# Kernel optimization log

Measured on AMD Instinct MI355X. Metric: run time of the kernel, lower is better.

The kernel has to match this reference:

```python
import jax, jax.numpy as jnp
import numpy as np
from jax import lax

STRIDE = (1, 1)
PADDING = ((1, 1), (1, 1))  # stride=1, padding=1 for 3x3 conv


def setup_inputs() -> dict:
    key = jax.random.key(0)
    k1, k2 = jax.random.split(key)
    x = jax.random.normal(k1, (16, 32, 224, 224), dtype=jnp.float32)
    # kaiming_normal_(mode='fan_out', nonlinearity='relu'): std = sqrt(2/fan_out)
    fan_out = 32 * 3 * 3
    weight = jax.random.normal(k2, (32, 32, 3, 3), dtype=jnp.float32) * np.sqrt(2.0 / fan_out)
    return {"x": x, "weight": weight}


def reference(x, weight):
    # absmax 8-bit activation fake-quant
    x_scale = jnp.abs(x).max() + 1e-5
    x_q = jnp.round(jnp.clip(x * 127.0 / x_scale, -128.0, 127.0))
    # BitNet b1.58 ternary weight fake-quant
    w_scale = jnp.abs(weight).mean() + 1e-5
    w_q = jnp.clip(jnp.round(weight / w_scale), -1.0, 1.0)
    # straight-through estimator (no-op in pure forward, kept for fidelity)
    w_ste = weight + lax.stop_gradient(w_q * w_scale - weight)
    x_ste = x + lax.stop_gradient(x_q * (x_scale / 127.0) - x)
    out = lax.conv_general_dilated(
        x_ste, w_ste,
        window_strides=STRIDE,
        padding=PADDING,
        dimension_numbers=("NCHW", "OIHW", "NCHW"),
    )
    return out
```

## Files before the change

kernel.cpp:

```cpp
#include <hip/hip_runtime.h>


typedef __attribute__((ext_vector_type(8))) short short8;
typedef __attribute__((ext_vector_type(4))) float f32x4;

#define HW    224
#define NCH   32
#define PLANE (HW * HW)
#define TH 16
#define TW 32

__device__ __forceinline__ int lds_h(int pix, int c) {
    int sw = (pix & 3) ^ ((pix >> 2) & 3);
    return pix * 32 + (c & 7) + ((((c >> 3) ^ sw) & 3) << 3);
}


__global__ __launch_bounds__(256) void absmax_kernel(const float* __restrict__ x,
                                                     unsigned* __restrict__ slots, int n4)
{
    const float4* x4 = (const float4*)x;
    float m = 0.f;
    int stride = gridDim.x * blockDim.x;
    for (int i = blockIdx.x * blockDim.x + threadIdx.x; i < n4; i += stride) {
        float4 v = x4[i];
        m = fmaxf(m, fmaxf(fmaxf(fabsf(v.x), fabsf(v.y)),
                           fmaxf(fabsf(v.z), fabsf(v.w))));
    }
    #pragma unroll
    for (int off = 32; off > 0; off >>= 1)
        m = fmaxf(m, __shfl_xor(m, off));
    __shared__ float wm[4];
    int lane = threadIdx.x & 63, wv = threadIdx.x >> 6;
    if (lane == 0) wm[wv] = m;
    __syncthreads();
    if (threadIdx.x == 0) {
        m = fmaxf(fmaxf(wm[0], wm[1]), fmaxf(wm[2], wm[3]));
        slots[blockIdx.x] = __float_as_uint(m);
    }
}

__global__ __launch_bounds__(256) void prep_kernel(const float* __restrict__ w,
                                                   const unsigned* __restrict__ slots,
                                                   float* __restrict__ scal,
                                                   unsigned short* __restrict__ wbuf)
{
    float s = 0.f;
    for (int i = threadIdx.x; i < 9216; i += 256) s += fabsf(w[i]);
    float m = 0.f;
    for (int i = threadIdx.x; i < 2048; i += 256)
        m = fmaxf(m, __uint_as_float(slots[i]));
    #pragma unroll
    for (int off = 32; off > 0; off >>= 1) {
        s += __shfl_xor(s, off);
        m = fmaxf(m, __shfl_xor(m, off));
    }
    __shared__ float sm[4], mm[4];
    __shared__ float s_ws;
    int lane = threadIdx.x & 63, wv = threadIdx.x >> 6;
    if (lane == 0) { sm[wv] = s; mm[wv] = m; }
    __syncthreads();
    if (threadIdx.x == 0) {
        float wscale = (sm[0] + sm[1] + sm[2] + sm[3]) / 9216.f + 1e-5f;
        float xscale = fmaxf(fmaxf(mm[0], mm[1]), fmaxf(mm[2], mm[3])) + 1e-5f;
        scal[0] = (xscale / 127.f) * wscale;
        scal[1] = 127.f / xscale;
        s_ws = wscale;
    }
    __syncthreads();
    float wscale = s_ws;
    for (int o = threadIdx.x; o < 9216; o += 256) {
        int frag = o >> 9, rem = o & 511;
        int l = rem >> 3, j = rem & 7;
        int tap = frag >> 1, kb = frag & 1;
        int kout = kb * 16 + (l & 15);
        int c = ((l >> 4) << 3) + j;
        int r = tap / 3, ss = tap % 3;
        float wv2 = w[((kout * 32 + c) * 3 + r) * 3 + ss];
        float q = fminf(1.f, fmaxf(-1.f, rintf(wv2 / wscale)));
        wbuf[o] = (unsigned short)(__float_as_uint(q) >> 16);
    }
}

__global__ __launch_bounds__(512, 4) void conv_kernel(const float* __restrict__ x,
                                                      const unsigned short* __restrict__ wbuf,
                                                      const float* __restrict__ scal,
                                                      float* __restrict__ out)
{
    __shared__ __align__(16) unsigned short xs[612 * 32];

    int bid = (blockIdx.x & 7) * 196 + (blockIdx.x >> 3);
    int tw = bid % 7;
    int rest = bid / 7;
    int th = rest % 14;
    int n  = rest / 14;
    int h0 = th * TH, w0 = tw * TW;

    int tid = threadIdx.x;
    int lane = tid & 63, wv = tid >> 6;

    float inv = scal[1];
    const float* xn = x + n * (NCH * PLANE);

    const short8* wfp = (const short8*)wbuf;
    short8 wa = wfp[lane];
    short8 wb = wfp[64 + lane];

    int slot = tid & 7;
    int c = (tid >> 3) & 31;
    int half = tid >> 8;
    const float* tb = xn + c * PLANE + w0 + slot * 4;
    int pixb = 1 + slot * 4;
    int hbase = half * 9;

    float4 v[9];
    float invr[9];
    #pragma unroll
    for (int i = 0; i < 9; ++i) {
        int gh = h0 - 1 + hbase + i;
        int ghc = gh < 0 ? 0 : (gh > HW - 1 ? HW - 1 : gh);
        invr[i] = (gh == ghc) ? inv : 0.f;
        v[i] = *(const float4*)(tb + ghc * HW);
    }
    float hv[3];
    #pragma unroll
    for (int it = 0; it < 3; ++it) {
        int e = tid + it * 512;
        hv[it] = 0.f;
        if (e < 1152) {
            int side = e & 1;
            int cc = (e >> 1) & 31;
            int hp = e >> 6;
            int gh = h0 - 1 + hp;
            int gw = side ? (w0 + TW) : (w0 - 1);
            int ghc = gh < 0 ? 0 : (gh > HW - 1 ? HW - 1 : gh);
            int gwc = gw < 0 ? 0 : (gw > HW - 1 ? HW - 1 : gw);
            float vv = xn[cc * PLANE + ghc * HW + gwc];
            hv[it] = (gh == ghc && gw == gwc) ? vv * inv : 0.f;
        }
    }
    #pragma unroll
    for (int i = 0; i < 9; ++i) {
        int p0 = (hbase + i) * 34 + pixb;
        float q0 = rintf(fminf(127.f, fmaxf(-128.f, v[i].x * invr[i])));
        float q1 = rintf(fminf(127.f, fmaxf(-128.f, v[i].y * invr[i])));
        float q2 = rintf(fminf(127.f, fmaxf(-128.f, v[i].z * invr[i])));
        float q3 = rintf(fminf(127.f, fmaxf(-128.f, v[i].w * invr[i])));
        xs[lds_h(p0 + 0, c)] = (unsigned short)(__float_as_uint(q0) >> 16);
        xs[lds_h(p0 + 1, c)] = (unsigned short)(__float_as_uint(q1) >> 16);
        xs[lds_h(p0 + 2, c)] = (unsigned short)(__float_as_uint(q2) >> 16);
        xs[lds_h(p0 + 3, c)] = (unsigned short)(__float_as_uint(q3) >> 16);
    }
    #pragma unroll
    for (int it = 0; it < 3; ++it) {
        int e = tid + it * 512;
        if (e < 1152) {
            int side = e & 1;
            int cc = (e >> 1) & 31;
            int hp = e >> 6;
            float q = rintf(fminf(127.f, fmaxf(-128.f, hv[it])));
            xs[lds_h(hp * 34 + (side ? 33 : 0), cc)] =
                (unsigned short)(__float_as_uint(q) >> 16);
        }
    }
    __syncthreads();

    int ln = lane & 15, cb = lane >> 4;
    f32x4 acc[2][2][2] = {};

    for (int tap = 0; tap < 9; ++tap) {
        short8 na, nb;
        if (tap < 8) {
            na = wfp[(2 * tap + 2) * 64 + lane];
            nb = wfp[(2 * tap + 3) * 64 + lane];
        }
        int r = tap / 3;
        int s2 = tap - r * 3;
        #pragma unroll
        for (int ri = 0; ri < 2; ++ri) {
            #pragma unroll
            for (int pb = 0; pb < 2; ++pb) {
                int pix = (wv * 2 + ri + r) * 34 + pb * 16 + ln + s2;
                int sw = (pix & 3) ^ ((pix >> 2) & 3);
                const short8 a = *(const short8*)&xs[pix * 32 + (((cb ^ sw) & 3) << 3)];
                acc[ri][pb][0] = __builtin_amdgcn_mfma_f32_16x16x32_bf16(
                    a, wa, acc[ri][pb][0], 0, 0, 0);
                acc[ri][pb][1] = __builtin_amdgcn_mfma_f32_16x16x32_bf16(
                    a, wb, acc[ri][pb][1], 0, 0, 0);
            }
        }
        wa = na;
        wb = nb;
    }

    float osc = scal[0];
    float* on = out + n * (NCH * PLANE);
    #pragma unroll
    for (int ri = 0; ri < 2; ++ri) {
        int h = h0 + wv * 2 + ri;
        #pragma unroll
        for (int pb = 0; pb < 2; ++pb) {
            int wcol = w0 + pb * 16 + cb * 4;
            #pragma unroll
            for (int kb = 0; kb < 2; ++kb) {
                int k = kb * 16 + ln;
                f32x4 o;
                o[0] = acc[ri][pb][kb][0] * osc;
                o[1] = acc[ri][pb][kb][1] * osc;
                o[2] = acc[ri][pb][kb][2] * osc;
                o[3] = acc[ri][pb][kb][3] * osc;
                *(f32x4*)&on[(k * HW + h) * HW + wcol] = o;
            }
        }
    }
}

extern "C" void kernel_launch(void* const* d_in, const int* in_sizes, int n_in,
                              void* d_out, int out_size, void* d_ws, size_t ws_size,
                              hipStream_t stream)
{
    const float* x = (const float*)d_in[0];
    const float* w = (const float*)d_in[1];
    float* outp = (float*)d_out;
    unsigned* slots = (unsigned*)d_ws;
    float* scal = (float*)((char*)d_ws + 8192);
    unsigned short* wbuf = (unsigned short*)((char*)d_ws + 8448);

    int n4 = (16 * NCH * PLANE) / 4;
    absmax_kernel<<<2048, 256, 0, stream>>>(x, slots, n4);
    prep_kernel<<<1, 256, 0, stream>>>(w, slots, scal, wbuf);
    conv_kernel<<<16 * 14 * 7, 512, 0, stream>>>(x, wbuf, scal, outp);
}
```

Before: 87.87 us.

## Fold prep kernel into absmax and conv, process two row tiles per block

Removes the single-block prep kernel. Weight quantization now runs in an extra block of the absmax launch, and the final 2048-slot max reduction moves into every conv block. Each conv block now handles two 16-row tiles instead of one, which halves the grid. The global loads for the second tile are issued during the first tile's MFMA work to hide latency. The cost is a redundant slot reduction in every block and fewer, longer blocks.

Result: slower. 121.7 us (+38.5%).

```diff
diff --git a/kernel.cpp b/kernel.cpp
--- a/kernel.cpp
+++ b/kernel.cpp
@@ -17,12 +17,48 @@
 
 
 __global__ __launch_bounds__(256) void absmax_kernel(const float* __restrict__ x,
-                                                     unsigned* __restrict__ slots, int n4)
+                                                     const float* __restrict__ w,
+                                                     unsigned* __restrict__ slots,
+                                                     float* __restrict__ scal,
+                                                     unsigned short* __restrict__ wbuf,
+                                                     int n4)
 {
+    int tid = threadIdx.x;
+    int lane = tid & 63, wv = tid >> 6;
+
+    if (blockIdx.x == 2048) {
+        float s = 0.f;
+        for (int i = tid; i < 9216; i += 256) s += fabsf(w[i]);
+        #pragma unroll
+        for (int off = 32; off > 0; off >>= 1) s += __shfl_xor(s, off);
+        __shared__ float sm[4];
+        __shared__ float s_ws;
+        if (lane == 0) sm[wv] = s;
+        __syncthreads();
+        if (tid == 0) {
+            float wscale = (sm[0] + sm[1] + sm[2] + sm[3]) / 9216.f + 1e-5f;
+            scal[0] = wscale;
+            s_ws = wscale;
+        }
+        __syncthreads();
+        float wscale = s_ws;
+        for (int o = tid; o < 9216; o += 256) {
+            int frag = o >> 9, rem = o & 511;
+            int l = rem >> 3, j = rem & 7;
+            int tap = frag >> 1, kb = frag & 1;
+            int kout = kb * 16 + (l & 15);
+            int c = ((l >> 4) << 3) + j;
+            int r = tap / 3, ss = tap % 3;
+            float wv2 = w[((kout * 32 + c) * 3 + r) * 3 + ss];
+            float q = fminf(1.f, fmaxf(-1.f, rintf(wv2 / wscale)));
+            wbuf[o] = (unsigned short)(__float_as_uint(q) >> 16);
+        }
+        return;
+    }
+
     const float4* x4 = (const float4*)x;
     float m = 0.f;
-    int stride = gridDim.x * blockDim.x;
-    for (int i = blockIdx.x * blockDim.x + threadIdx.x; i < n4; i += stride) {
+    for (int i = blockIdx.x * 256 + tid; i < n4; i += 2048 * 256) {
         float4 v = x4[i];
         m = fmaxf(m, fmaxf(fmaxf(fabsf(v.x), fabsf(v.y)),
                            fmaxf(fabsf(v.z), fabsf(v.w))));
@@ -31,80 +67,36 @@
     for (int off = 32; off > 0; off >>= 1)
         m = fmaxf(m, __shfl_xor(m, off));
     __shared__ float wm[4];
-    int lane = threadIdx.x & 63, wv = threadIdx.x >> 6;
     if (lane == 0) wm[wv] = m;
     __syncthreads();
-    if (threadIdx.x == 0) {
+    if (tid == 0) {
         m = fmaxf(fmaxf(wm[0], wm[1]), fmaxf(wm[2], wm[3]));
         slots[blockIdx.x] = __float_as_uint(m);
     }
 }
 
-__global__ __launch_bounds__(256) void prep_kernel(const float* __restrict__ w,
-                                                   const unsigned* __restrict__ slots,
-                                                   float* __restrict__ scal,
-                                                   unsigned short* __restrict__ wbuf)
-{
-    float s = 0.f;
-    for (int i = threadIdx.x; i < 9216; i += 256) s += fabsf(w[i]);
-    float m = 0.f;
-    for (int i = threadIdx.x; i < 2048; i += 256)
-        m = fmaxf(m, __uint_as_float(slots[i]));
-    #pragma unroll
-    for (int off = 32; off > 0; off >>= 1) {
-        s += __shfl_xor(s, off);
-        m = fmaxf(m, __shfl_xor(m, off));
-    }
-    __shared__ float sm[4], mm[4];
-    __shared__ float s_ws;
-    int lane = threadIdx.x & 63, wv = threadIdx.x >> 6;
-    if (lane == 0) { sm[wv] = s; mm[wv] = m; }
-    __syncthreads();
-    if (threadIdx.x == 0) {
-        float wscale = (sm[0] + sm[1] + sm[2] + sm[3]) / 9216.f + 1e-5f;
-        float xscale = fmaxf(fmaxf(mm[0], mm[1]), fmaxf(mm[2], mm[3])) + 1e-5f;
-        scal[0] = (xscale / 127.f) * wscale;
-        scal[1] = 127.f / xscale;
-        s_ws = wscale;
-    }
-    __syncthreads();
-    float wscale = s_ws;
-    for (int o = threadIdx.x; o < 9216; o += 256) {
-        int frag = o >> 9, rem = o & 511;
-        int l = rem >> 3, j = rem & 7;
-        int tap = frag >> 1, kb = frag & 1;
-        int kout = kb * 16 + (l & 15);
-        int c = ((l >> 4) << 3) + j;
-        int r = tap / 3, ss = tap % 3;
-        float wv2 = w[((kout * 32 + c) * 3 + r) * 3 + ss];
-        float q = fminf(1.f, fmaxf(-1.f, rintf(wv2 / wscale)));
-        wbuf[o] = (unsigned short)(__float_as_uint(q) >> 16);
-    }
-}
-
 __global__ __launch_bounds__(512, 4) void conv_kernel(const float* __restrict__ x,
                                                       const unsigned short* __restrict__ wbuf,
+                                                      const unsigned* __restrict__ slots,
                                                       const float* __restrict__ scal,
                                                       float* __restrict__ out)
 {
     __shared__ __align__(16) unsigned short xs[612 * 32];
-
-    int bid = (blockIdx.x & 7) * 196 + (blockIdx.x >> 3);
+    __shared__ float sred[8];
+
+    int bid = (blockIdx.x & 7) * 98 + (blockIdx.x >> 3);
     int tw = bid % 7;
     int rest = bid / 7;
-    int th = rest % 14;
-    int n  = rest / 14;
-    int h0 = th * TH, w0 = tw * TW;
+    int qh = rest % 7;
+    int n  = rest / 7;
+    int w0 = tw * TW;
 
     int tid = threadIdx.x;
     int lane = tid & 63, wv = tid >> 6;
 
-    float inv = scal[1];
     const float* xn = x + n * (NCH * PLANE);
-
+    float* on = out + n * (NCH * PLANE);
     const short8* wfp = (const short8*)wbuf;
-    short8 wa = wfp[lane];
-    short8 wb = wfp[64 + lane];
 
     int slot = tid & 7;
     int c = (tid >> 3) & 31;
@@ -113,105 +105,149 @@
     int pixb = 1 + slot * 4;
     int hbase = half * 9;
 
+    int h0 = qh * 32;
     float4 v[9];
-    float invr[9];
+    float hv[3];
     #pragma unroll
     for (int i = 0; i < 9; ++i) {
         int gh = h0 - 1 + hbase + i;
         int ghc = gh < 0 ? 0 : (gh > HW - 1 ? HW - 1 : gh);
-        invr[i] = (gh == ghc) ? inv : 0.f;
         v[i] = *(const float4*)(tb + ghc * HW);
     }
-    float hv[3];
     #pragma unroll
     for (int it = 0; it < 3; ++it) {
         int e = tid + it * 512;
         hv[it] = 0.f;
         if (e < 1152) {
-            int side = e & 1;
-            int cc = (e >> 1) & 31;
-            int hp = e >> 6;
+            int side = e & 1, cc = (e >> 1) & 31, hp = e >> 6;
             int gh = h0 - 1 + hp;
             int gw = side ? (w0 + TW) : (w0 - 1);
             int ghc = gh < 0 ? 0 : (gh > HW - 1 ? HW - 1 : gh);
             int gwc = gw < 0 ? 0 : (gw > HW - 1 ? HW - 1 : gw);
-            float vv = xn[cc * PLANE + ghc * HW + gwc];
-            hv[it] = (gh == ghc && gw == gwc) ? vv * inv : 0.f;
-        }
-    }
-    #pragma unroll
-    for (int i = 0; i < 9; ++i) {
-        int p0 = (hbase + i) * 34 + pixb;
-        float q0 = rintf(fminf(127.f, fmaxf(-128.f, v[i].x * invr[i])));
-        float q1 = rintf(fminf(127.f, fmaxf(-128.f, v[i].y * invr[i])));
-        float q2 = rintf(fminf(127.f, fmaxf(-128.f, v[i].z * invr[i])));
-        float q3 = rintf(fminf(127.f, fmaxf(-128.f, v[i].w * invr[i])));
-        xs[lds_h(p0 + 0, c)] = (unsigned short)(__float_as_uint(q0) >> 16);
-        xs[lds_h(p0 + 1, c)] = (unsigned short)(__float_as_uint(q1) >> 16);
-        xs[lds_h(p0 + 2, c)] = (unsigned short)(__float_as_uint(q2) >> 16);
-        xs[lds_h(p0 + 3, c)] = (unsigned short)(__float_as_uint(q3) >> 16);
-    }
-    #pragma unroll
-    for (int it = 0; it < 3; ++it) {
-        int e = tid + it * 512;
-        if (e < 1152) {
-            int side = e & 1;
-            int cc = (e >> 1) & 31;
-            int hp = e >> 6;
-            float q = rintf(fminf(127.f, fmaxf(-128.f, hv[it])));
-            xs[lds_h(hp * 34 + (side ? 33 : 0), cc)] =
-                (unsigned short)(__float_as_uint(q) >> 16);
-        }
-    }
+            hv[it] = xn[cc * PLANE + ghc * HW + gwc];
+        }
+    }
+
+    uint4 sv = ((const uint4*)slots)[tid];
+    float wscale = scal[0];
+    float m2 = fmaxf(fmaxf(__uint_as_float(sv.x), __uint_as_float(sv.y)),
+                     fmaxf(__uint_as_float(sv.z), __uint_as_float(sv.w)));
+    #pragma unroll
+    for (int off = 32; off > 0; off >>= 1)
+        m2 = fmaxf(m2, __shfl_xor(m2, off));
+    if (lane == 0) sred[wv] = m2;
     __syncthreads();
+    float xmax = fmaxf(fmaxf(fmaxf(sred[0], sred[1]), fmaxf(sred[2], sred[3])),
+                       fmaxf(fmaxf(sred[4], sred[5]), fmaxf(sred[6], sred[7])));
+    float xscale = xmax + 1e-5f;
+    float inv = 127.f / xscale;
+    float osc = (xscale / 127.f) * wscale;
 
     int ln = lane & 15, cb = lane >> 4;
-    f32x4 acc[2][2][2] = {};
-
-    for (int tap = 0; tap < 9; ++tap) {
-        short8 na, nb;
-        if (tap < 8) {
-            na = wfp[(2 * tap + 2) * 64 + lane];
-            nb = wfp[(2 * tap + 3) * 64 + lane];
-        }
-        int r = tap / 3;
-        int s2 = tap - r * 3;
+
+    #pragma unroll
+    for (int t = 0; t < 2; ++t) {
+        #pragma unroll
+        for (int i = 0; i < 9; ++i) {
+            int gh = h0 - 1 + hbase + i;
+            float vs = ((unsigned)gh < (unsigned)HW) ? inv : 0.f;
+            int p0 = (hbase + i) * 34 + pixb;
+            float q0 = rintf(fminf(127.f, fmaxf(-128.f, v[i].x * vs)));
+            float q1 = rintf(fminf(127.f, fmaxf(-128.f, v[i].y * vs)));
+            float q2 = rintf(fminf(127.f, fmaxf(-128.f, v[i].z * vs)));
+            float q3 = rintf(fminf(127.f, fmaxf(-128.f, v[i].w * vs)));
+            xs[lds_h(p0 + 0, c)] = (unsigned short)(__float_as_uint(q0) >> 16);
+            xs[lds_h(p0 + 1, c)] = (unsigned short)(__float_as_uint(q1) >> 16);
+            xs[lds_h(p0 + 2, c)] = (unsigned short)(__float_as_uint(q2) >> 16);
+            xs[lds_h(p0 + 3, c)] = (unsigned short)(__float_as_uint(q3) >> 16);
+        }
+        #pragma unroll
+        for (int it = 0; it < 3; ++it) {
+            int e = tid + it * 512;
+            if (e < 1152) {
+                int side = e & 1, cc = (e >> 1) & 31, hp = e >> 6;
+                int gh = h0 - 1 + hp;
+                int gw = side ? (w0 + TW) : (w0 - 1);
+                float vs = ((unsigned)gh < (unsigned)HW && (unsigned)gw < (unsigned)HW)
+                               ? inv : 0.f;
+                float q = rintf(fminf(127.f, fmaxf(-128.f, hv[it] * vs)));
+                xs[lds_h(hp * 34 + (side ? 33 : 0), cc)] =
+                    (unsigned short)(__float_as_uint(q) >> 16);
+            }
+        }
+        __syncthreads();
+
+        f32x4 acc[2][2][2] = {};
+        short8 wa = wfp[lane];
+        short8 wb = wfp[64 + lane];
+        for (int tap = 0; tap < 9; ++tap) {
+            short8 na, nb;
+            if (tap < 8) {
+                na = wfp[(2 * tap + 2) * 64 + lane];
+                nb = wfp[(2 * tap + 3) * 64 + lane];
+            }
+            int r = tap / 3;
+            int s2 = tap - r * 3;
+            #pragma unroll
+            for (int ri = 0; ri < 2; ++ri) {
+                #pragma unroll
+                for (int pb = 0; pb < 2; ++pb) {
+                    int pix = (wv * 2 + ri + r) * 34 + pb * 16 + ln + s2;
+                    int sw = (pix & 3) ^ ((pix >> 2) & 3);
+                    const short8 a = *(const short8*)&xs[pix * 32 + (((cb ^ sw) & 3) << 3)];
+                    acc[ri][pb][0] = __builtin_amdgcn_mfma_f32_16x16x32_bf16(
+                        a, wa, acc[ri][pb][0], 0, 0, 0);
+                    acc[ri][pb][1] = __builtin_amdgcn_mfma_f32_16x16x32_bf16(
+                        a, wb, acc[ri][pb][1], 0, 0, 0);
+                }
+            }
+            wa = na;
+            wb = nb;
+        }
+
+        if (t == 0) {
+            int h1 = h0 + TH;
+            #pragma unroll
+            for (int i = 0; i < 9; ++i) {
+                int gh = h1 - 1 + hbase + i;
+                int ghc = gh < 0 ? 0 : (gh > HW - 1 ? HW - 1 : gh);
+                v[i] = *(const float4*)(tb + ghc * HW);
+            }
+            #pragma unroll
+            for (int it = 0; it < 3; ++it) {
+                int e = tid + it * 512;
+                if (e < 1152) {
+                    int side = e & 1, cc = (e >> 1) & 31, hp = e >> 6;
+                    int gh = h1 - 1 + hp;
+                    int gw = side ? (w0 + TW) : (w0 - 1);
+                    int ghc = gh < 0 ? 0 : (gh > HW - 1 ? HW - 1 : gh);
+                    int gwc = gw < 0 ? 0 : (gw > HW - 1 ? HW - 1 : gw);
+                    hv[it] = xn[cc * PLANE + ghc * HW + gwc];
+                }
+            }
+        }
+
         #pragma unroll
         for (int ri = 0; ri < 2; ++ri) {
+            int h = h0 + wv * 2 + ri;
             #pragma unroll
             for (int pb = 0; pb < 2; ++pb) {
-                int pix = (wv * 2 + ri + r) * 34 + pb * 16 + ln + s2;
-                int sw = (pix & 3) ^ ((pix >> 2) & 3);
-                const short8 a = *(const short8*)&xs[pix * 32 + (((cb ^ sw) & 3) << 3)];
-                acc[ri][pb][0] = __builtin_amdgcn_mfma_f32_16x16x32_bf16(
-                    a, wa, acc[ri][pb][0], 0, 0, 0);
-                acc[ri][pb][1] = __builtin_amdgcn_mfma_f32_16x16x32_bf16(
-                    a, wb, acc[ri][pb][1], 0, 0, 0);
-            }
-        }
-        wa = na;
-        wb = nb;
-    }
-
-    float osc = scal[0];
-    float* on = out + n * (NCH * PLANE);
-    #pragma unroll
-    for (int ri = 0; ri < 2; ++ri) {
-        int h = h0 + wv * 2 + ri;
-        #pragma unroll
-        for (int pb = 0; pb < 2; ++pb) {
-            int wcol = w0 + pb * 16 + cb * 4;
-            #pragma unroll
-            for (int kb = 0; kb < 2; ++kb) {
-                int k = kb * 16 + ln;
-                f32x4 o;
-                o[0] = acc[ri][pb][kb][0] * osc;
-                o[1] = acc[ri][pb][kb][1] * osc;
-                o[2] = acc[ri][pb][kb][2] * osc;
-                o[3] = acc[ri][pb][kb][3] * osc;
-                *(f32x4*)&on[(k * HW + h) * HW + wcol] = o;
-            }
-        }
+                int wcol = w0 + pb * 16 + cb * 4;
+                #pragma unroll
+                for (int kb = 0; kb < 2; ++kb) {
+                    int k = kb * 16 + ln;
+                    f32x4 o;
+                    o[0] = acc[ri][pb][kb][0] * osc;
+                    o[1] = acc[ri][pb][kb][1] * osc;
+                    o[2] = acc[ri][pb][kb][2] * osc;
+                    o[3] = acc[ri][pb][kb][3] * osc;
+                    *(f32x4*)&on[(k * HW + h) * HW + wcol] = o;
+                }
+            }
+        }
+
+        h0 += TH;
+        if (t == 0) __syncthreads();
     }
 }
 
@@ -227,7 +263,6 @@
     unsigned short* wbuf = (unsigned short*)((char*)d_ws + 8448);
 
     int n4 = (16 * NCH * PLANE) / 4;
-    absmax_kernel<<<2048, 256, 0, stream>>>(x, slots, n4);
-    prep_kernel<<<1, 256, 0, stream>>>(w, slots, scal, wbuf);
-    conv_kernel<<<16 * 14 * 7, 512, 0, stream>>>(x, wbuf, scal, outp);
-}
+    absmax_kernel<<<2049, 256, 0, stream>>>(x, w, slots, scal, wbuf, n4);
+    conv_kernel<<<784, 512, 0, stream>>>(x, wbuf, slots, scal, outp);
+}
```
